# Optimization experiments

Hardware: AMD Instinct MI355X
Metric: run time of the kernel (lower is better)

The kernel has to match this reference:

```python
import math
import jax, jax.numpy as jnp
from jax import lax
import numpy as np

SPARSITY = 0.05
EMBEDDING_SIZE = 2048
BATCH = 32768


def setup_inputs() -> dict:
    key = jax.random.key(0)
    k0, k1, k2 = jax.random.split(key, 3)
    x = jax.random.normal(k0, (BATCH, 28, 28), dtype=jnp.float32)
    # conv: out=5, in=1, k=3, no bias (kaiming-ish scale)
    conv_w = jax.random.normal(k1, (5, 1, 3, 3), dtype=jnp.float32) * (1.0 / math.sqrt(9))
    bn_gamma = jnp.ones((5,), jnp.float32)
    bn_beta = jnp.zeros((5,), jnp.float32)
    bn_mean = jnp.zeros((5,), jnp.float32)
    bn_var = jnp.ones((5,), jnp.float32)
    # fc: [EMBEDDING_SIZE, 320], no bias
    fc_w = jax.random.normal(k2, (EMBEDDING_SIZE, 5 * 8 * 8), dtype=jnp.float32) * (1.0 / math.sqrt(320))
    return {"x": x, "conv_w": conv_w, "bn_gamma": bn_gamma, "bn_beta": bn_beta,
            "bn_mean": bn_mean, "bn_var": bn_var, "fc_w": fc_w}


def _kwta(z):
    # k-winners-take-all: top k_active entries per row -> 1, rest -> 0.
    k_active = math.ceil(SPARSITY * z.shape[1])
    topv, _ = lax.top_k(z, k_active)          # [B, k]
    thr = topv[:, -1:]                         # kth largest per row
    binary = (z >= thr).astype(z.dtype)
    # straight-through: forward = binary, backward = identity
    return z + lax.stop_gradient(binary - z)


def reference(x, conv_w, bn_gamma, bn_beta, bn_mean, bn_var, fc_w):
    h = x[:, None, :, :]  # [B,1,28,28]
    h = lax.conv_general_dilated(h, conv_w, window_strides=(1, 1), padding="VALID",
                                 dimension_numbers=("NCHW", "OIHW", "NCHW"))  # [B,5,26,26]
    inv_std = bn_gamma / jnp.sqrt(bn_var + 1e-5)
    h = (h - bn_mean[None, :, None, None]) * inv_std[None, :, None, None] + bn_beta[None, :, None, None]
    h = jnp.maximum(h, 0.0)
    # max_pool2d(kernel=3, stride=3), floor mode -> [B,5,8,8]
    h = lax.reduce_window(h, -jnp.inf, lax.max, (1, 1, 3, 3), (1, 1, 3, 3), "VALID")
    h = h.reshape(h.shape[0], -1)              # [B,320]
    z = h @ fc_w.T                             # [B,EMBEDDING_SIZE]
    return _kwta(z)
```

## Files before the change

kernel.cpp:

```cpp
#include <hip/hip_runtime.h>
#include <math.h>

#define BATCH 32768
#define EMB   2048
#define KDIM  320
#define KACT  103

#define BM 16
#define GTHREADS 512

#define CIMG 8

__global__ __launch_bounds__(256) void transpose_w_kernel(const float* __restrict__ W,
                                                          float* __restrict__ WT) {
  __shared__ float tile[32][33];
  const int k0 = blockIdx.x * 32;
  const int n0 = blockIdx.y * 32;
  const int tx = threadIdx.x;
  const int ty = threadIdx.y;
  for (int i = ty; i < 32; i += 8)
    tile[i][tx] = W[(size_t)(n0 + i) * KDIM + k0 + tx];
  __syncthreads();
  for (int i = ty; i < 32; i += 8)
    WT[(size_t)(k0 + i) * EMB + n0 + tx] = tile[tx][i];
}

__global__ __launch_bounds__(512) void conv_pool_kernel(const float* __restrict__ x,
                                                        const float* __restrict__ cw,
                                                        const float* __restrict__ gamma,
                                                        const float* __restrict__ beta,
                                                        const float* __restrict__ mean,
                                                        const float* __restrict__ var,
                                                        float* __restrict__ H) {
#pragma clang fp contract(off)
  __shared__ float xs[CIMG * 784];
  __shared__ float wv[45];
  __shared__ float inv_s[5], mu_s[5], be_s[5];
  const int t  = threadIdx.x;
  const int b0 = blockIdx.x * CIMG;

  {
    const float4* src = (const float4*)(x + (size_t)b0 * 784);
    float4* dst = (float4*)xs;
    for (int i = t; i < CIMG * 196; i += 512) dst[i] = src[i];
  }
  if (t < 45) wv[t] = cw[t];
  if (t < 5) {
    inv_s[t] = gamma[t] / sqrtf(var[t] + 1e-5f);
    mu_s[t] = mean[t];
    be_s[t] = beta[t];
  }
  __syncthreads();

  const int img  = t >> 6;
  const int lane = t & 63;
  const int py = lane >> 3;
  const int px = lane & 7;
  const float* xb = xs + img * 784;

  float xr[5][5];
#pragma unroll
  for (int i = 0; i < 5; ++i)
#pragma unroll
    for (int j = 0; j < 5; ++j)
      xr[i][j] = xb[(3 * py + i) * 28 + 3 * px + j];

  float wr[45];
#pragma unroll
  for (int i = 0; i < 45; ++i) wr[i] = wv[i];

  float res[5];
#pragma unroll
  for (int c = 0; c < 5; ++c) {
    const float inv = inv_s[c], mu = mu_s[c], be = be_s[c];
    float mx = -__builtin_huge_valf();
#pragma unroll
    for (int ry = 0; ry < 3; ++ry)
#pragma unroll
      for (int rx = 0; rx < 3; ++rx) {
        float s = 0.0f;
#pragma unroll
        for (int di = 0; di < 3; ++di)
#pragma unroll
          for (int dj = 0; dj < 3; ++dj)
            s = __builtin_fmaf(xr[ry + di][rx + dj], wr[c * 9 + di * 3 + dj], s);
        float t1 = s - mu;
        float t2 = t1 * inv;
        float t3 = t2 + be;
        mx = fmaxf(mx, t3);
      }
    res[c] = fmaxf(mx, 0.0f);
  }

#pragma unroll
  for (int c = 0; c < 5; ++c)
    H[(size_t)(b0 + img) * KDIM + c * 64 + lane] = res[c];
}

__global__ __launch_bounds__(GTHREADS) void gemm_topk_kernel(const float* __restrict__ H,
                                                             const float* __restrict__ WT,
                                                             float* __restrict__ out) {
  __shared__ __align__(16) float As[KDIM * BM];
  __shared__ unsigned prefix_s[BM];
  __shared__ unsigned rank_s[BM];
  unsigned* histo = (unsigned*)As;

  const int t    = threadIdx.x;
  const int lane = t & 63;
  const int w    = t >> 6;
  const int m0   = blockIdx.x * BM;
  const int nt   = t * 4;

  for (int i = t; i < KDIM * BM; i += GTHREADS) {
    const int m = i / KDIM;
    const int k = i - m * KDIM;
    As[k * BM + m] = H[(size_t)(m0 + m) * KDIM + k];
  }
  if (t < BM) { prefix_s[t] = 0u; rank_s[t] = KACT; }
  __syncthreads();

  float acc[BM][4];
#pragma unroll
  for (int m = 0; m < BM; ++m)
#pragma unroll
    for (int j = 0; j < 4; ++j) acc[m][j] = 0.0f;

  const float* wp = WT + nt;
  float4 nb0 = *(const float4*)(wp + 0 * EMB);
  float4 nb1 = *(const float4*)(wp + 1 * EMB);
  float4 nb2 = *(const float4*)(wp + 2 * EMB);
  float4 nb3 = *(const float4*)(wp + 3 * EMB);

  for (int k4 = 0; k4 < KDIM / 4; ++k4) {
    const float4 b0 = nb0, b1 = nb1, b2 = nb2, b3 = nb3;
    if (k4 + 1 < KDIM / 4) {
      const float* wn = wp + (size_t)(k4 + 1) * 4 * EMB;
      nb0 = *(const float4*)(wn + 0 * EMB);
      nb1 = *(const float4*)(wn + 1 * EMB);
      nb2 = *(const float4*)(wn + 2 * EMB);
      nb3 = *(const float4*)(wn + 3 * EMB);
    }
#pragma unroll
    for (int kk = 0; kk < 4; ++kk) {
      const float4* ap = (const float4*)(As + (4 * k4 + kk) * BM);
      const float4 a0 = ap[0], a1 = ap[1], a2 = ap[2], a3 = ap[3];
      const float av[BM] = {a0.x, a0.y, a0.z, a0.w, a1.x, a1.y, a1.z, a1.w,
                            a2.x, a2.y, a2.z, a2.w, a3.x, a3.y, a3.z, a3.w};
      const float4 bb = (kk == 0) ? b0 : (kk == 1) ? b1 : (kk == 2) ? b2 : b3;
#pragma unroll
      for (int m = 0; m < BM; ++m) {
        acc[m][0] = __builtin_fmaf(av[m], bb.x, acc[m][0]);
        acc[m][1] = __builtin_fmaf(av[m], bb.y, acc[m][1]);
        acc[m][2] = __builtin_fmaf(av[m], bb.z, acc[m][2]);
        acc[m][3] = __builtin_fmaf(av[m], bb.w, acc[m][3]);
      }
    }
  }
  __syncthreads();

  for (int pass = 0; pass < 4; ++pass) {
    const int shift = 24 - pass * 8;
    for (int i = t; i < BM * 256; i += GTHREADS) histo[i] = 0u;
    unsigned pref[BM];
#pragma unroll
    for (int m = 0; m < BM; ++m) pref[m] = prefix_s[m];
    __syncthreads();
#pragma unroll
    for (int m = 0; m < BM; ++m) {
#pragma unroll
      for (int j = 0; j < 4; ++j) {
        unsigned u = __float_as_uint(acc[m][j]);
        u = (u & 0x80000000u) ? ~u : (u | 0x80000000u);
        const bool in = (pass == 0) || ((u >> (shift + 8)) == pref[m]);
        if (in) atomicAdd(&histo[m * 256 + ((u >> shift) & 255u)], 1u);
      }
    }
    __syncthreads();
    for (int rr = 0; rr < 2; ++rr) {
      const int m = w * 2 + rr;
      const unsigned rank = rank_s[m];
      const uint4 c = *(const uint4*)(histo + m * 256 + lane * 4);
      const unsigned s = c.x + c.y + c.z + c.w;
      unsigned suf = s;
#pragma unroll
      for (int off = 1; off < 64; off <<= 1) {
        const unsigned o = __shfl_down(suf, off);
        if (lane + off < 64) suf += o;
      }
      const unsigned above = suf - s;
      if (above < rank && rank <= suf) {
        unsigned bin, newr;
        if (above + c.w >= rank)                    { bin = lane * 4 + 3; newr = rank - above; }
        else if (above + c.w + c.z >= rank)         { bin = lane * 4 + 2; newr = rank - above - c.w; }
        else if (above + c.w + c.z + c.y >= rank)   { bin = lane * 4 + 1; newr = rank - above - c.w - c.z; }
        else                                        { bin = lane * 4 + 0; newr = rank - above - c.w - c.z - c.y; }
        prefix_s[m] = (prefix_s[m] << 8) | bin;
        rank_s[m] = newr;
      }
    }
    __syncthreads();
  }

  unsigned thr[BM];
#pragma unroll
  for (int m = 0; m < BM; ++m) thr[m] = prefix_s[m];

#pragma unroll
  for (int m = 0; m < BM; ++m) {
    float4 o;
    float* op = (float*)&o;
#pragma unroll
    for (int j = 0; j < 4; ++j) {
      unsigned u = __float_as_uint(acc[m][j]);
      u = (u & 0x80000000u) ? ~u : (u | 0x80000000u);
      op[j] = (u >= thr[m]) ? 1.0f : 0.0f;
    }
    *(float4*)(out + (size_t)(m0 + m) * EMB + nt) = o;
  }
}

extern "C" void kernel_launch(void* const* d_in, const int* in_sizes, int n_in,
                              void* d_out, int out_size, void* d_ws, size_t ws_size,
                              hipStream_t stream) {
  const float* x      = (const float*)d_in[0];
  const float* conv_w = (const float*)d_in[1];
  const float* gamma  = (const float*)d_in[2];
  const float* beta   = (const float*)d_in[3];
  const float* mean   = (const float*)d_in[4];
  const float* var    = (const float*)d_in[5];
  const float* fc_w   = (const float*)d_in[6];
  float* out = (float*)d_out;

  float* H  = (float*)d_ws;
  float* WT = (float*)d_ws + (size_t)BATCH * KDIM;

  transpose_w_kernel<<<dim3(KDIM / 32, EMB / 32), dim3(32, 8), 0, stream>>>(fc_w, WT);
  conv_pool_kernel<<<BATCH / CIMG, 512, 0, stream>>>(x, conv_w, gamma, beta, mean, var, H);
  gemm_topk_kernel<<<BATCH / BM, GTHREADS, 0, stream>>>(H, WT, out);
}
```

Baseline: 996.2 us.

## Store pooled features K-major so GEMM reads A directly from global

The conv/pool kernel now handles 16 images per block, stages results in shared memory and writes the feature matrix transposed (K-major, batch contiguous). The GEMM kernel drops its shared-memory staging and transpose of A and instead loads 16 contiguous floats per k directly from global memory, uniform across the block. This removes a barrier and the strided shared-memory transpose in the GEMM. The cost is a transpose inside the conv kernel, and the GEMM's A loads now go through global memory or cache inside the inner loop, which may add latency.

```diff
diff --git a/kernel.cpp b/kernel.cpp
--- a/kernel.cpp
+++ b/kernel.cpp
@@ -9,7 +9,7 @@
 #define BM 16
 #define GTHREADS 512
 
-#define CIMG 8
+#define CIMG 16
 
 __global__ __launch_bounds__(256) void transpose_w_kernel(const float* __restrict__ W,
                                                           float* __restrict__ WT) {
@@ -31,9 +31,10 @@
                                                         const float* __restrict__ beta,
                                                         const float* __restrict__ mean,
                                                         const float* __restrict__ var,
-                                                        float* __restrict__ H) {
+                                                        float* __restrict__ Ht) {
 #pragma clang fp contract(off)
   __shared__ float xs[CIMG * 784];
+  __shared__ float hs[KDIM * 17];
   __shared__ float wv[45];
   __shared__ float inv_s[5], mu_s[5], be_s[5];
   const int t  = threadIdx.x;
@@ -52,58 +53,62 @@
   }
   __syncthreads();
 
-  const int img  = t >> 6;
+  const int i0   = t >> 6;
   const int lane = t & 63;
   const int py = lane >> 3;
   const int px = lane & 7;
-  const float* xb = xs + img * 784;
-
-  float xr[5][5];
-#pragma unroll
-  for (int i = 0; i < 5; ++i)
-#pragma unroll
-    for (int j = 0; j < 5; ++j)
-      xr[i][j] = xb[(3 * py + i) * 28 + 3 * px + j];
-
-  float wr[45];
-#pragma unroll
-  for (int i = 0; i < 45; ++i) wr[i] = wv[i];
-
-  float res[5];
-#pragma unroll
-  for (int c = 0; c < 5; ++c) {
-    const float inv = inv_s[c], mu = mu_s[c], be = be_s[c];
-    float mx = -__builtin_huge_valf();
-#pragma unroll
-    for (int ry = 0; ry < 3; ++ry)
-#pragma unroll
-      for (int rx = 0; rx < 3; ++rx) {
-        float s = 0.0f;
-#pragma unroll
-        for (int di = 0; di < 3; ++di)
-#pragma unroll
-          for (int dj = 0; dj < 3; ++dj)
-            s = __builtin_fmaf(xr[ry + di][rx + dj], wr[c * 9 + di * 3 + dj], s);
-        float t1 = s - mu;
-        float t2 = t1 * inv;
-        float t3 = t2 + be;
-        mx = fmaxf(mx, t3);
-      }
-    res[c] = fmaxf(mx, 0.0f);
-  }
-
-#pragma unroll
-  for (int c = 0; c < 5; ++c)
-    H[(size_t)(b0 + img) * KDIM + c * 64 + lane] = res[c];
-}
-
-__global__ __launch_bounds__(GTHREADS) void gemm_topk_kernel(const float* __restrict__ H,
+
+  for (int ii = 0; ii < 2; ++ii) {
+    const int img = i0 * 2 + ii;
+    const float* xb = xs + img * 784;
+
+    float xr[5][5];
+#pragma unroll
+    for (int i = 0; i < 5; ++i)
+#pragma unroll
+      for (int j = 0; j < 5; ++j)
+        xr[i][j] = xb[(3 * py + i) * 28 + 3 * px + j];
+
+#pragma unroll
+    for (int c = 0; c < 5; ++c) {
+      float wr[9];
+#pragma unroll
+      for (int i = 0; i < 9; ++i) wr[i] = wv[c * 9 + i];
+      const float inv = inv_s[c], mu = mu_s[c], be = be_s[c];
+      float mx = -__builtin_huge_valf();
+#pragma unroll
+      for (int ry = 0; ry < 3; ++ry)
+#pragma unroll
+        for (int rx = 0; rx < 3; ++rx) {
+          float s = 0.0f;
+#pragma unroll
+          for (int di = 0; di < 3; ++di)
+#pragma unroll
+            for (int dj = 0; dj < 3; ++dj)
+              s = __builtin_fmaf(xr[ry + di][rx + dj], wr[di * 3 + dj], s);
+          float t1 = s - mu;
+          float t2 = t1 * inv;
+          float t3 = t2 + be;
+          mx = fmaxf(mx, t3);
+        }
+      hs[(c * 64 + lane) * 17 + img] = fmaxf(mx, 0.0f);
+    }
+  }
+  __syncthreads();
+
+  for (int idx = t; idx < KDIM * CIMG; idx += 512) {
+    const int k = idx >> 4;
+    const int img = idx & 15;
+    Ht[(size_t)k * BATCH + b0 + img] = hs[k * 17 + img];
+  }
+}
+
+__global__ __launch_bounds__(GTHREADS) void gemm_topk_kernel(const float* __restrict__ Ht,
                                                              const float* __restrict__ WT,
                                                              float* __restrict__ out) {
-  __shared__ __align__(16) float As[KDIM * BM];
+  __shared__ unsigned histo[BM * 256];
   __shared__ unsigned prefix_s[BM];
   __shared__ unsigned rank_s[BM];
-  unsigned* histo = (unsigned*)As;
 
   const int t    = threadIdx.x;
   const int lane = t & 63;
@@ -111,13 +116,7 @@
   const int m0   = blockIdx.x * BM;
   const int nt   = t * 4;
 
-  for (int i = t; i < KDIM * BM; i += GTHREADS) {
-    const int m = i / KDIM;
-    const int k = i - m * KDIM;
-    As[k * BM + m] = H[(size_t)(m0 + m) * KDIM + k];
-  }
   if (t < BM) { prefix_s[t] = 0u; rank_s[t] = KACT; }
-  __syncthreads();
 
   float acc[BM][4];
 #pragma unroll
@@ -125,6 +124,7 @@
 #pragma unroll
     for (int j = 0; j < 4; ++j) acc[m][j] = 0.0f;
 
+  const float* Ap = Ht + m0;
   const float* wp = WT + nt;
   float4 nb0 = *(const float4*)(wp + 0 * EMB);
   float4 nb1 = *(const float4*)(wp + 1 * EMB);
@@ -142,10 +142,10 @@
     }
 #pragma unroll
     for (int kk = 0; kk < 4; ++kk) {
-      const float4* ap = (const float4*)(As + (4 * k4 + kk) * BM);
-      const float4 a0 = ap[0], a1 = ap[1], a2 = ap[2], a3 = ap[3];
-      const float av[BM] = {a0.x, a0.y, a0.z, a0.w, a1.x, a1.y, a1.z, a1.w,
-                            a2.x, a2.y, a2.z, a2.w, a3.x, a3.y, a3.z, a3.w};
+      const float* ak = Ap + (size_t)(4 * k4 + kk) * BATCH;
+      float av[BM];
+#pragma unroll
+      for (int m = 0; m < BM; ++m) av[m] = ak[m];
       const float4 bb = (kk == 0) ? b0 : (kk == 1) ? b1 : (kk == 2) ? b2 : b3;
 #pragma unroll
       for (int m = 0; m < BM; ++m) {
@@ -231,10 +231,10 @@
   const float* fc_w   = (const float*)d_in[6];
   float* out = (float*)d_out;
 
-  float* H  = (float*)d_ws;
-  float* WT = (float*)d_ws + (size_t)BATCH * KDIM;
+  float* Ht = (float*)d_ws;
+  float* WT = (float*)d_ws + (size_t)KDIM * BATCH;
 
   transpose_w_kernel<<<dim3(KDIM / 32, EMB / 32), dim3(32, 8), 0, stream>>>(fc_w, WT);
-  conv_pool_kernel<<<BATCH / CIMG, 512, 0, stream>>>(x, conv_w, gamma, beta, mean, var, H);
-  gemm_topk_kernel<<<BATCH / BM, GTHREADS, 0, stream>>>(H, WT, out);
-}
+  conv_pool_kernel<<<BATCH / CIMG, 512, 0, stream>>>(x, conv_w, gamma, beta, mean, var, Ht);
+  gemm_topk_kernel<<<BATCH / BM, GTHREADS, 0, stream>>>(Ht, WT, out);
+}
```

After: 854.4 us. 1.17x faster.
